# Performance work log

Measured on AMD Instinct MI355X. Metric: run time of the kernel, lower is better.

## Reference

```python
import jax, jax.numpy as jnp
import numpy as np

P = 256      # identities
K = 16       # instances per identity per modality
C = 4096     # feature dim
MARGIN = 0.6 # margin_euc


def setup_inputs() -> dict:
    key = jax.random.key(0)
    x = jax.random.normal(key, (2 * P * K, C), dtype=jnp.float32)
    half = jnp.repeat(jnp.arange(P, dtype=jnp.int64), K)
    pids = jnp.concatenate([half, half])
    return {"x": x, "pids": pids}


def reference(x, pids):
    n = x.shape[0]          # 2*P*K
    twop = 2 * P
    # hierarchy-center features: mean over the K instances of each (modality, id) group
    pidhc = pids.reshape(twop, -1)[:, 0]                    # [2P]
    hcen = x.reshape(twop, -1, C).mean(axis=1)              # [2P, C]
    # euclidean distance matrix [N, 2P]
    d2 = ((x * x).sum(axis=1, keepdims=True)
          + (hcen * hcen).sum(axis=1)[None, :]
          - 2.0 * (x @ hcen.T))
    dist = jnp.sqrt(jnp.clip(d2, 1e-12))
    mask = pids[:, None] == pidhc[None, :]                  # same-identity mask

    # loss1: cross-modal positive pull. Rows in first half (modality 0) match
    # centers in second column half (modality 1 centers), and vice versa.
    row_first = (jnp.arange(n) < n // 2)[:, None]           # [N,1]
    col_second = (jnp.arange(twop) >= P)[None, :]           # [1,2P]
    sel = mask & (row_first == col_second)
    loss1 = jnp.sum(jnp.where(sel, dist, 0.0)) / jnp.sum(sel).astype(dist.dtype)

    # loss2: margin push on all non-matching centers
    neg = ~mask
    hinge = jnp.maximum(MARGIN - dist, 0.0)
    loss2 = jnp.sum(jnp.where(neg, hinge, 0.0)) / jnp.sum(neg).astype(dist.dtype)

    return loss1 + loss2
```

## Files before the change

kernel.cpp:

```cpp
#include <hip/hip_runtime.h>
#include <math.h>

#define P_    256
#define K_    16
#define C4_   1024
#define N_    8192
#define TWOP  512
#define NSL   8
#define NTAILB 32
#define MARGIN_F 0.6f
#define EXCAP   8192
#define FLAGCAP 16384

__device__ __forceinline__ float wave_reduce_f(float v) {
    #pragma unroll
    for (int o = 32; o > 0; o >>= 1) v += __shfl_xor(v, o, 64);
    return v;
}

__device__ __forceinline__ void bfly16(float val[16], const int lane) {
    #define BFLY_STAGE(MASK, HALF)                                          \
    {                                                                       \
        const bool upper = (lane & MASK) != 0;                              \
        _Pragma("unroll")                                                   \
        for (int i = 0; i < HALF; ++i) {                                    \
            const float send = upper ? val[i] : val[i + HALF];              \
            const float recv = __shfl_xor(send, MASK, 64);                  \
            val[i] = (upper ? val[i + HALF] : val[i]) + recv;               \
        }                                                                   \
    }
    BFLY_STAGE(1, 8)
    BFLY_STAGE(2, 4)
    BFLY_STAGE(4, 2)
    BFLY_STAGE(8, 1)
    #undef BFLY_STAGE
    val[0] += __shfl_xor(val[0], 16, 64);
    val[0] += __shfl_xor(val[0], 32, 64);
}

__global__ __launch_bounds__(256) void k_fused(const float* __restrict__ x,
                                               float* __restrict__ dot_part,
                                               float* __restrict__ sq_part,
                                               float* __restrict__ hn2_part,
                                               unsigned* __restrict__ counters) {
    const int blk = blockIdx.x;
    const int p = blk >> 3;
    const int s = blk & (NSL - 1);
    const int t = threadIdx.x;
    const int lane = t & 63;
    const int wv = t >> 6;
    const int side = wv >> 1, whalf = wv & 1;

    if (blk == 0 && t < 4) counters[t] = 0u;

    __shared__ float4 cen[2][128];

    const float4* x4 = (const float4*)x;
    const int grp = side ? (P_ + p) : p;
    const size_t base0 = ((size_t)grp * K_) * C4_ + s * 128 + whalf * 64 + lane;

    float4 v[16];
    #pragma unroll
    for (int r = 0; r < 16; ++r) v[r] = x4[base0 + (size_t)r * C4_];

    float4 cs = {0.f, 0.f, 0.f, 0.f};
    float sq[16];
    #pragma unroll
    for (int r = 0; r < 16; ++r) {
        cs.x += v[r].x; cs.y += v[r].y; cs.z += v[r].z; cs.w += v[r].w;
        sq[r] = v[r].x*v[r].x + v[r].y*v[r].y + v[r].z*v[r].z + v[r].w*v[r].w;
    }
    cen[side][whalf * 64 + lane] = cs;

    float h2 = cs.x*cs.x + cs.y*cs.y + cs.z*cs.z + cs.w*cs.w;
    h2 = wave_reduce_f(h2);
    if (lane == 0) hn2_part[(p * NSL + s) * 4 + wv] = h2;

    __syncthreads();

    const float4 hp = cen[side ^ 1][whalf * 64 + lane];
    float dp[16];
    #pragma unroll
    for (int r = 0; r < 16; ++r)
        dp[r] = v[r].x*hp.x + v[r].y*hp.y + v[r].z*hp.z + v[r].w*hp.w;

    bfly16(dp, lane);
    bfly16(sq, lane);

    if (lane < 16) {
        const int idx = ((lane & 1) << 3) | ((lane & 2) << 1)
                      | ((lane & 4) >> 1) | ((lane & 8) >> 3);
        const int ob = (p * NSL + s) * 64 + wv * 16 + idx;
        dot_part[ob] = dp[0];
        sq_part [ob] = sq[0];
    }
}

__global__ __launch_bounds__(256) void k_tail(const float* __restrict__ x,
                                              const float* __restrict__ dot_part,
                                              const float* __restrict__ sq_part,
                                              const float* __restrict__ hn2_part,
                                              const int* __restrict__ pids,
                                              float* __restrict__ s1part,
                                              unsigned* __restrict__ c1part,
                                              unsigned* __restrict__ negpart,
                                              unsigned* __restrict__ counters,
                                              int* __restrict__ extralist,
                                              int* __restrict__ flaglist,
                                              float* __restrict__ out) {
    __shared__ int   gp[TWOP];
    __shared__ float shn[TWOP], sh2[TWOP];
    __shared__ int   s_ok, sLast;
    __shared__ float smin[4], smax[4];
    __shared__ float rf[4];
    __shared__ unsigned ru[4], rn[4];
    __shared__ float bc_s1, bc_c1, bc_ng;
    const int t = threadIdx.x;
    const int lane = t & 63, wv = t >> 6;

    if (t == 0) s_ok = 1;
    __syncthreads();

    float lmin = 3.0e38f, lmax = -3.0e38f;
    for (int j = t; j < TWOP; j += 256) {
        const int g = pids[j * K_];
        gp[j] = g;
        if (g != (j & (P_ - 1))) s_ok = 0;
        const int side = (j < P_) ? 0 : 1;
        const int pp = j & (P_ - 1);
        float a = 0.f;
        #pragma unroll
        for (int ss = 0; ss < NSL; ++ss) {
            a += hn2_part[(pp * NSL + ss) * 4 + side * 2];
            a += hn2_part[(pp * NSL + ss) * 4 + side * 2 + 1];
        }
        a *= (1.0f / 256.0f);
        sh2[j] = a;
        const float r = sqrtf(a);
        shn[j] = r;
        lmin = fminf(lmin, r); lmax = fmaxf(lmax, r);
    }
    #pragma unroll
    for (int o = 32; o > 0; o >>= 1) {
        lmin = fminf(lmin, __shfl_xor(lmin, o, 64));
        lmax = fmaxf(lmax, __shfl_xor(lmax, o, 64));
    }
    if (lane == 0) { smin[wv] = lmin; smax[wv] = lmax; }
    __syncthreads();
    const float hmin = fminf(fminf(smin[0], smin[1]), fminf(smin[2], smin[3]));
    const float hmax = fmaxf(fmaxf(smax[0], smax[1]), fmaxf(smax[2], smax[3]));
    const int structured = s_ok;

    const int gr  = blockIdx.x * 256 + t;
    const int grp = gr >> 4, kk = gr & 15;
    const int pp2 = grp & (P_ - 1);
    const int sideR = (grp < P_) ? 0 : 1;
    const int pg  = (grp < P_) ? (P_ + pp2) : pp2;

    float dot = 0.f, sq = 0.f;
    #pragma unroll
    for (int ss = 0; ss < NSL; ++ss) {
        const int sb = (pp2 * NSL + ss) * 64 + sideR * 32 + kk;
        dot += dot_part[sb] + dot_part[sb + 16];
        sq  += sq_part [sb] + sq_part [sb + 16];
    }
    const float dist = sqrtf(fmaxf(sq + sh2[pg] - 0.125f * dot, 1e-12f));
    const float myxn = sqrtf(sq);
    const int mypid = pids[gr];
    const bool window_clear = (myxn >= hmax + MARGIN_F) || (myxn <= hmin - MARGIN_F);

    unsigned mall, mopp;
    if (structured && mypid == pp2 && window_clear) {
        mall = 2u; mopp = 1u;
    } else {
        const int jb = (gr < N_ / 2) ? P_ : 0;
        mall = 0u; mopp = 0u;
        for (int j = 0; j < TWOP; ++j) {
            if (gp[j] == mypid) {
                ++mall;
                if (j >= jb && j < jb + P_) {
                    ++mopp;
                    if (j != pg) {
                        unsigned s0 = atomicAdd(&counters[0], 1u);
                        if (s0 < EXCAP) extralist[s0] = gr * TWOP + j;
                        else atomicExch(&counters[2], 1u);
                    }
                }
            } else if (fabsf(myxn - shn[j]) < MARGIN_F) {
                unsigned s0 = atomicAdd(&counters[1], 1u);
                if (s0 < FLAGCAP) flaglist[s0] = gr * TWOP + j;
                else atomicExch(&counters[2], 1u);
            }
        }
    }

    float s1 = (gp[pg] == mypid) ? dist : 0.f;
    unsigned neg = (unsigned)TWOP - mall;
    unsigned mo = mopp;
    #pragma unroll
    for (int o = 32; o > 0; o >>= 1) {
        s1  += __shfl_xor(s1, o, 64);
        mo  += __shfl_xor(mo, o, 64);
        neg += __shfl_xor(neg, o, 64);
    }
    if (lane == 0) { rf[wv] = s1; ru[wv] = mo; rn[wv] = neg; }
    __syncthreads();
    if (t == 0) {
        atomicExch(&s1part[blockIdx.x],  rf[0] + rf[1] + rf[2] + rf[3]);
        atomicExch(&c1part[blockIdx.x],  ru[0] + ru[1] + ru[2] + ru[3]);
        atomicExch(&negpart[blockIdx.x], rn[0] + rn[1] + rn[2] + rn[3]);
    }

    __threadfence();
    if (t == 0) {
        const unsigned n = atomicAdd(&counters[3], 1u);
        sLast = (n == NTAILB - 1) ? 1 : 0;
    }
    __syncthreads();
    if (!sLast) return;
    __threadfence();

    {
        float s1v = 0.f; unsigned c1v = 0u, ngv = 0u;
        if (t < NTAILB) { s1v = s1part[t]; c1v = c1part[t]; ngv = negpart[t]; }
        if (t < 64) {
            #pragma unroll
            for (int o = 32; o > 0; o >>= 1) {
                s1v += __shfl_xor(s1v, o, 64);
                c1v += __shfl_xor(c1v, o, 64);
                ngv += __shfl_xor(ngv, o, 64);
            }
            if (t == 0) { bc_s1 = s1v; bc_c1 = (float)c1v; bc_ng = (float)ngv; }
        }
    }
    __syncthreads();

    unsigned ne = counters[0]; if (ne > EXCAP)   ne = EXCAP;
    unsigned nf = counters[1]; if (nf > FLAGCAP) nf = FLAGCAP;
    float s1x = 0.f, l2 = 0.f;
    const float4* x4 = (const float4*)x;
    for (unsigned u = 0; u < ne + nf; ++u) {
        const bool isex = (u < ne);
        const int code = isex ? extralist[u] : flaglist[u - ne];
        const int i = code >> 9, jj = code & (TWOP - 1);
        const float4* xr = x4 + (size_t)i * C4_;
        const float4* gb = x4 + (size_t)jj * K_ * C4_;
        float dpv = 0.f, sqi = 0.f;
        for (int c = t; c < C4_; c += 256) {
            const float4 a = xr[c];
            float hx = 0.f, hy = 0.f, hz = 0.f, hw = 0.f;
            #pragma unroll
            for (int rr = 0; rr < K_; ++rr) {
                const float4 u4 = gb[(size_t)rr * C4_ + c];
                hx += u4.x; hy += u4.y; hz += u4.z; hw += u4.w;
            }
            dpv += (a.x*hx + a.y*hy + a.z*hz + a.w*hw) * 0.0625f;
            sqi += a.x*a.x + a.y*a.y + a.z*a.z + a.w*a.w;
        }
        #pragma unroll
        for (int o = 32; o > 0; o >>= 1) {
            dpv += __shfl_xor(dpv, o, 64);
            sqi += __shfl_xor(sqi, o, 64);
        }
        if (lane == 0) { rf[wv] = dpv; smin[wv] = sqi; }
        __syncthreads();
        if (t == 0) {
            const float ddot = rf[0] + rf[1] + rf[2] + rf[3];
            const float sqv  = smin[0] + smin[1] + smin[2] + smin[3];
            const float d2 = sqv + sh2[jj] - 2.0f * ddot;
            const float dist2 = sqrtf(fmaxf(d2, 1e-12f));
            if (isex) s1x += dist2;
            else { const float h = MARGIN_F - dist2; if (h > 0.f) l2 += h; }
        }
        __syncthreads();
    }

    if (t == 0) out[0] = (bc_s1 + s1x) / bc_c1 + l2 / bc_ng;
}

extern "C" void kernel_launch(void* const* d_in, const int* in_sizes, int n_in,
                              void* d_out, int out_size, void* d_ws, size_t ws_size,
                              hipStream_t stream) {
    const float* x    = (const float*)d_in[0];
    const int*   pids = (const int*)d_in[1];

    float* ws = (float*)d_ws;
    float*    dot_part = ws;
    float*    sq_part  = dot_part + P_ * NSL * 64;
    float*    hn2_part = sq_part + P_ * NSL * 64;
    float*    s1part   = hn2_part + P_ * NSL * 4;
    unsigned* c1part   = (unsigned*)(s1part + NTAILB);
    unsigned* negpart  = c1part + NTAILB;
    unsigned* counters = negpart + NTAILB;
    int*      extralist= (int*)(counters + 4);
    int*      flaglist = extralist + EXCAP;

    hipLaunchKernelGGL(k_fused, dim3(P_ * NSL), dim3(256), 0, stream,
                       x, dot_part, sq_part, hn2_part, counters);
    hipLaunchKernelGGL(k_tail,  dim3(NTAILB),   dim3(256), 0, stream,
                       x, dot_part, sq_part, hn2_part, pids,
                       s1part, c1part, negpart, counters,
                       extralist, flaglist, (float*)d_out);
}
```

Measured before the change: 35.22 us.

## Halve block size and have each wave process two column slices

```diff
diff --git a/kernel.cpp b/kernel.cpp
--- a/kernel.cpp
+++ b/kernel.cpp
@@ -6,7 +6,7 @@
 #define C4_   1024
 #define N_    8192
 #define TWOP  512
-#define NSL   8
+#define NSL   16
 #define NTAILB 32
 #define MARGIN_F 0.6f
 #define EXCAP   8192
@@ -38,62 +38,94 @@
     val[0] += __shfl_xor(val[0], 32, 64);
 }
 
-__global__ __launch_bounds__(256) void k_fused(const float* __restrict__ x,
+__device__ __forceinline__ int bitrev4(const int m) {
+    return ((m & 1) << 3) | ((m & 2) << 1) | ((m & 4) >> 1) | ((m & 8) >> 3);
+}
+
+__device__ __forceinline__ void barrier_lds_only() {
+    asm volatile("s_waitcnt lgkmcnt(0)\n\ts_barrier" ::: "memory");
+}
+
+__global__ __launch_bounds__(128) void k_fused(const float* __restrict__ x,
                                                float* __restrict__ dot_part,
                                                float* __restrict__ sq_part,
                                                float* __restrict__ hn2_part,
                                                unsigned* __restrict__ counters) {
     const int blk = blockIdx.x;
     const int p = blk >> 3;
-    const int s = blk & (NSL - 1);
+    const int sp = blk & 7;
     const int t = threadIdx.x;
     const int lane = t & 63;
-    const int wv = t >> 6;
-    const int side = wv >> 1, whalf = wv & 1;
+    const int side = t >> 6;
 
     if (blk == 0 && t < 4) counters[t] = 0u;
 
-    __shared__ float4 cen[2][128];
+    __shared__ float4 cen[2][2][64];
 
     const float4* x4 = (const float4*)x;
     const int grp = side ? (P_ + p) : p;
-    const size_t base0 = ((size_t)grp * K_) * C4_ + s * 128 + whalf * 64 + lane;
-
-    float4 v[16];
-    #pragma unroll
-    for (int r = 0; r < 16; ++r) v[r] = x4[base0 + (size_t)r * C4_];
-
-    float4 cs = {0.f, 0.f, 0.f, 0.f};
-    float sq[16];
+    const size_t rowbase = (size_t)grp * K_ * C4_;
+    const int colA = sp * 64 + lane;
+    const int colB = (sp + 8) * 64 + lane;
+
+    float4 vA[16], vB[16];
+    #pragma unroll
+    for (int r = 0; r < 16; ++r) vA[r] = x4[rowbase + (size_t)r * C4_ + colA];
+    #pragma unroll
+    for (int r = 0; r < 16; ++r) vB[r] = x4[rowbase + (size_t)r * C4_ + colB];
+
+    float4 csA = {0.f, 0.f, 0.f, 0.f};
+    float sqA[16];
     #pragma unroll
     for (int r = 0; r < 16; ++r) {
-        cs.x += v[r].x; cs.y += v[r].y; cs.z += v[r].z; cs.w += v[r].w;
-        sq[r] = v[r].x*v[r].x + v[r].y*v[r].y + v[r].z*v[r].z + v[r].w*v[r].w;
-    }
-    cen[side][whalf * 64 + lane] = cs;
-
-    float h2 = cs.x*cs.x + cs.y*cs.y + cs.z*cs.z + cs.w*cs.w;
-    h2 = wave_reduce_f(h2);
-    if (lane == 0) hn2_part[(p * NSL + s) * 4 + wv] = h2;
-
-    __syncthreads();
-
-    const float4 hp = cen[side ^ 1][whalf * 64 + lane];
-    float dp[16];
+        csA.x += vA[r].x; csA.y += vA[r].y; csA.z += vA[r].z; csA.w += vA[r].w;
+        sqA[r] = vA[r].x*vA[r].x + vA[r].y*vA[r].y + vA[r].z*vA[r].z + vA[r].w*vA[r].w;
+    }
+    bfly16(sqA, lane);
+    const int obA = ((p * NSL + sp) * 2 + side) * 16;
+    if (lane < 16) sq_part[obA + bitrev4(lane)] = sqA[0];
+
+    cen[0][side][lane] = csA;
+    float h2A = csA.x*csA.x + csA.y*csA.y + csA.z*csA.z + csA.w*csA.w;
+    h2A = wave_reduce_f(h2A);
+    if (lane == 0) hn2_part[(p * NSL + sp) * 2 + side] = h2A;
+
+    barrier_lds_only();
+
+    const float4 hpA = cen[0][side ^ 1][lane];
+    float dpA[16];
     #pragma unroll
     for (int r = 0; r < 16; ++r)
-        dp[r] = v[r].x*hp.x + v[r].y*hp.y + v[r].z*hp.z + v[r].w*hp.w;
-
-    bfly16(dp, lane);
-    bfly16(sq, lane);
-
-    if (lane < 16) {
-        const int idx = ((lane & 1) << 3) | ((lane & 2) << 1)
-                      | ((lane & 4) >> 1) | ((lane & 8) >> 3);
-        const int ob = (p * NSL + s) * 64 + wv * 16 + idx;
-        dot_part[ob] = dp[0];
-        sq_part [ob] = sq[0];
-    }
+        dpA[r] = vA[r].x*hpA.x + vA[r].y*hpA.y + vA[r].z*hpA.z + vA[r].w*hpA.w;
+    bfly16(dpA, lane);
+    if (lane < 16) dot_part[obA + bitrev4(lane)] = dpA[0];
+
+    float4 csB = {0.f, 0.f, 0.f, 0.f};
+    float sqB[16];
+    #pragma unroll
+    for (int r = 0; r < 16; ++r) {
+        csB.x += vB[r].x; csB.y += vB[r].y; csB.z += vB[r].z; csB.w += vB[r].w;
+        sqB[r] = vB[r].x*vB[r].x + vB[r].y*vB[r].y + vB[r].z*vB[r].z + vB[r].w*vB[r].w;
+    }
+    bfly16(sqB, lane);
+    const int sB = sp + 8;
+    const int obB = ((p * NSL + sB) * 2 + side) * 16;
+    if (lane < 16) sq_part[obB + bitrev4(lane)] = sqB[0];
+
+    cen[1][side][lane] = csB;
+    float h2B = csB.x*csB.x + csB.y*csB.y + csB.z*csB.z + csB.w*csB.w;
+    h2B = wave_reduce_f(h2B);
+    if (lane == 0) hn2_part[(p * NSL + sB) * 2 + side] = h2B;
+
+    barrier_lds_only();
+
+    const float4 hpB = cen[1][side ^ 1][lane];
+    float dpB[16];
+    #pragma unroll
+    for (int r = 0; r < 16; ++r)
+        dpB[r] = vB[r].x*hpB.x + vB[r].y*hpB.y + vB[r].z*hpB.z + vB[r].w*hpB.w;
+    bfly16(dpB, lane);
+    if (lane < 16) dot_part[obB + bitrev4(lane)] = dpB[0];
 }
 
 __global__ __launch_bounds__(256) void k_tail(const float* __restrict__ x,
@@ -130,10 +162,8 @@
         const int pp = j & (P_ - 1);
         float a = 0.f;
         #pragma unroll
-        for (int ss = 0; ss < NSL; ++ss) {
-            a += hn2_part[(pp * NSL + ss) * 4 + side * 2];
-            a += hn2_part[(pp * NSL + ss) * 4 + side * 2 + 1];
-        }
+        for (int ss = 0; ss < NSL; ++ss)
+            a += hn2_part[(pp * NSL + ss) * 2 + side];
         a *= (1.0f / 256.0f);
         sh2[j] = a;
         const float r = sqrtf(a);
@@ -160,9 +190,9 @@
     float dot = 0.f, sq = 0.f;
     #pragma unroll
     for (int ss = 0; ss < NSL; ++ss) {
-        const int sb = (pp2 * NSL + ss) * 64 + sideR * 32 + kk;
-        dot += dot_part[sb] + dot_part[sb + 16];
-        sq  += sq_part [sb] + sq_part [sb + 16];
+        const int sb = ((pp2 * NSL + ss) * 2 + sideR) * 16 + kk;
+        dot += dot_part[sb];
+        sq  += sq_part [sb];
     }
     const float dist = sqrtf(fmaxf(sq + sh2[pg] - 0.125f * dot, 1e-12f));
     const float myxn = sqrtf(sq);
@@ -286,18 +316,18 @@
 
     float* ws = (float*)d_ws;
     float*    dot_part = ws;
-    float*    sq_part  = dot_part + P_ * NSL * 64;
-    float*    hn2_part = sq_part + P_ * NSL * 64;
-    float*    s1part   = hn2_part + P_ * NSL * 4;
+    float*    sq_part  = dot_part + P_ * NSL * 32;
+    float*    hn2_part = sq_part + P_ * NSL * 32;
+    float*    s1part   = hn2_part + P_ * NSL * 2;
     unsigned* c1part   = (unsigned*)(s1part + NTAILB);
     unsigned* negpart  = c1part + NTAILB;
     unsigned* counters = negpart + NTAILB;
     int*      extralist= (int*)(counters + 4);
     int*      flaglist = extralist + EXCAP;
 
-    hipLaunchKernelGGL(k_fused, dim3(P_ * NSL), dim3(256), 0, stream,
+    hipLaunchKernelGGL(k_fused, dim3(P_ * 8), dim3(128), 0, stream,
                        x, dot_part, sq_part, hn2_part, counters);
-    hipLaunchKernelGGL(k_tail,  dim3(NTAILB),   dim3(256), 0, stream,
+    hipLaunchKernelGGL(k_tail,  dim3(NTAILB), dim3(256), 0, stream,
                        x, dot_part, sq_part, hn2_part, pids,
                        s1part, c1part, negpart, counters,
                        extralist, flaglist, (float*)d_out);
```

Result: slower. 38.87 us (+10.4%).
